# Kernel optimization log

Measured on AMD Instinct MI355X. Metric: run time of the kernel, lower is better.

The kernel has to match this reference:

```python
import jax, jax.numpy as jnp
import numpy as np
from jax import lax

NPOINT = 1024
RADIUS = 0.4
NSAMPLE = 32
EPS = 1e-5


def setup_inputs() -> dict:
    key = jax.random.key(0)
    ks = jax.random.split(key, 8)
    B, N, Cin = 16, 4096, 64
    mlp = [64, 64, 128]
    last = Cin + 3
    inp = {
        "xyz": jax.random.normal(ks[0], (B, N, 3), dtype=jnp.float32),
        "points": jax.random.normal(ks[1], (B, N, Cin), dtype=jnp.float32),
    }
    for i, co in enumerate(mlp):
        inp[f"w{i}"] = jax.random.normal(ks[2 + i], (co, last), dtype=jnp.float32) * 0.05
        inp[f"b{i}"] = jnp.zeros((co,), jnp.float32)
        inp[f"g{i}"] = jnp.ones((co,), jnp.float32)
        inp[f"be{i}"] = jnp.zeros((co,), jnp.float32)
        last = co
    return inp


def _gather(pts, idx):
    # pts: [B, N, C], idx: [B, ...] -> [B, ..., C]
    return jax.vmap(lambda p, i: p[i])(pts, idx)


def farthest_point_sample(xyz, npoint):
    # Deterministic variant: start from index 0 (torch uses a random start).
    B, N, _ = xyz.shape
    bidx = jnp.arange(B)

    def step(carry, _):
        distance, farthest = carry
        centroid = xyz[bidx, farthest][:, None, :]          # [B,1,3]
        dist = jnp.sum((xyz - centroid) ** 2, -1)           # [B,N]
        distance = jnp.minimum(distance, dist)
        return (distance, jnp.argmax(distance, -1)), farthest

    init = (jnp.full((B, N), 1e10, xyz.dtype), jnp.zeros((B,), jnp.int32))
    _, cent = lax.scan(step, init, None, length=npoint)
    return cent.T                                            # [B, npoint]


def query_ball_point(radius, nsample, xyz, new_xyz):
    B, N, _ = xyz.shape
    # [B, S, N] squared distances centroid -> all points
    sqr = jnp.sum((xyz[:, None, :, :] - new_xyz[:, :, None, :]) ** 2, -1)
    gi = jnp.where(sqr > radius ** 2, N, jnp.arange(N)[None, None, :])
    gi = jnp.sort(gi, axis=-1)[:, :, :nsample]               # smallest in-ball indices
    gi = jnp.where(gi == N, gi[:, :, :1], gi)                # pad with first neighbor
    return gi


def reference(xyz, points, w0, b0, g0, be0, w1, b1, g1, be1, w2, b2, g2, be2):
    B, N, _ = xyz.shape
    cent = farthest_point_sample(xyz, NPOINT)                # [B,S]
    new_xyz = _gather(xyz, cent)                             # [B,S,3]
    gi = query_ball_point(RADIUS, NSAMPLE, xyz, new_xyz)     # [B,S,K]
    grouped_xyz = _gather(xyz, gi) - new_xyz[:, :, None, :]  # [B,S,K,3]
    x = jnp.concatenate([grouped_xyz, _gather(points, gi)], -1)  # [B,S,K,3+Cin]
    for w, b, g, be in ((w0, b0, g0, be0), (w1, b1, g1, be1), (w2, b2, g2, be2)):
        x = jnp.einsum('bskc,oc->bsko', x, w) + b            # 1x1 conv
        m = jnp.mean(x, axis=(0, 1, 2))
        v = jnp.var(x, axis=(0, 1, 2))                       # biased var, as torch BN
        x = jax.nn.relu(g * (x - m) * lax.rsqrt(v + EPS) + be)
    new_points = jnp.max(x, axis=2)                          # max over nsample -> [B,S,Cout]
    return new_xyz, new_points
```

## Files before the change

### kernel.cpp

```cpp
#include <hip/hip_runtime.h>
#include <math.h>


static constexpr int BATCH  = 16;
static constexpr int NPTS   = 4096;
static constexpr int NPOINT = 1024;
static constexpr int NSAMP  = 32;
static constexpr int CIN    = 64;
static constexpr int ROWS   = BATCH * NPOINT * NSAMP;
static constexpr int NBLK   = ROWS / 64;

typedef unsigned long long u64;

__device__ __forceinline__ float sqdist(float x, float y, float z,
                                        float cx, float cy, float cz) {
    float dx = x - cx, dy = y - cy, dz = z - cz;
    return __fadd_rn(__fadd_rn(__fmul_rn(dx, dx), __fmul_rn(dy, dy)), __fmul_rn(dz, dz));
}

#if __has_builtin(__builtin_amdgcn_update_dpp) && __has_builtin(__builtin_amdgcn_readlane)
#define DPP_MAX(x, ctrl)                                                              \
    do {                                                                              \
        int _o = __builtin_amdgcn_update_dpp(__float_as_int(x), __float_as_int(x),    \
                                             (ctrl), 0xf, 0xf, false);                \
        (x) = fmaxf((x), __int_as_float(_o));                                         \
    } while (0)
__device__ __forceinline__ float wave_max_f32(float v) {
    DPP_MAX(v, 0x111);
    DPP_MAX(v, 0x112);
    DPP_MAX(v, 0x114);
    DPP_MAX(v, 0x118);
    DPP_MAX(v, 0x142);
    DPP_MAX(v, 0x143);
    return __int_as_float(__builtin_amdgcn_readlane(__float_as_int(v), 63));
}
#else
__device__ __forceinline__ float wave_max_f32(float v) {
#pragma unroll
    for (int m = 1; m < 64; m <<= 1) v = fmaxf(v, __shfl_xor(v, m));
    return v;
}
#endif

__global__ __launch_bounds__(512) void pre_kernel(
    const float* __restrict__ xyz, const float* __restrict__ points,
    const float* __restrict__ w0, const float* __restrict__ b0,
    float* __restrict__ P, float* __restrict__ new_xyz) {
    __shared__ __align__(16) char s_raw[53376];
    const int tid = threadIdx.x;

    if (blockIdx.x < 16) {
        float2* sxy  = (float2*)s_raw;
        float*  szv  = (float*)(s_raw + 32768);
        int*    s_cent = (int*)(s_raw + 49152);
        u64*    s_red  = (u64*)(s_raw + 53248);

        const int b = blockIdx.x;
        const float* xb = xyz + (size_t)b * NPTS * 3;
        for (int p = tid; p < NPTS; p += 512) {
            sxy[p] = make_float2(xb[p * 3 + 0], xb[p * 3 + 1]);
            szv[p] = xb[p * 3 + 2];
        }
        __syncthreads();
        float px[8], py[8], pz[8], dist[8];
#pragma unroll
        for (int j = 0; j < 8; ++j) {
            int p = tid + j * 512;
            float2 f = sxy[p];
            px[j] = f.x; py[j] = f.y; pz[j] = szv[p];
            dist[j] = 1e10f;
        }
        const int lane = tid & 63, wid = tid >> 6;
        int far = 0;
        for (int it = 0; it < NPOINT; ++it) {
            if (tid == 0) s_cent[it] = far;
            const float2 cxy = sxy[far];
            const float  cz  = szv[far];
            float bv = -1.0f;
            int   bi = 0;
#pragma unroll
            for (int j = 0; j < 8; ++j) {
                float d  = sqdist(px[j], py[j], pz[j], cxy.x, cxy.y, cz);
                float nd = fminf(dist[j], d);
                dist[j]  = nd;
                if (nd > bv) { bv = nd; bi = tid + j * 512; }
            }
            float gmax = wave_max_f32(bv);
            u64 mask = __ballot(bv == gmax);
            int widx = __shfl(bi, (int)__builtin_ctzll(mask));
            if (lane == 0)
                s_red[(it & 1) * 8 + wid] =
                    ((u64)__float_as_uint(gmax) << 32) | (unsigned)(4095 - widx);
            __syncthreads();
            const u64* sr = &s_red[(it & 1) * 8];
            u64 w = sr[0];
#pragma unroll
            for (int k = 1; k < 8; ++k) { u64 o = sr[k]; w = (o > w) ? o : w; }
            far = 4095 - (int)(w & 0xffffffffu);
        }
        __syncthreads();
        for (int s = tid; s < NPOINT; s += 512) {
            int c = s_cent[s];
            float2 f = sxy[c];
            new_xyz[((size_t)b * NPOINT + s) * 3 + 0] = f.x;
            new_xyz[((size_t)b * NPOINT + s) * 3 + 1] = f.y;
            new_xyz[((size_t)b * NPOINT + s) * 3 + 2] = szv[c];
        }
    } else {
        float (*xw)[68] = (float(*)[68])s_raw;
        float (*wt)[68] = (float(*)[68])(s_raw + 34816);
        const int blk = blockIdx.x - 16;
        const int pt0 = blk * 128;
        const int ty = tid >> 4, tx = tid & 15;

        for (int idx = tid; idx < 128 * 3; idx += 512) {
            int r = idx / 3, d = idx - r * 3;
            xw[r][d] = xyz[(size_t)(pt0 + r) * 3 + d];
        }
        for (int idx = tid; idx < 128 * 16; idx += 512) {
            int r = idx >> 4, c4 = idx & 15;
            float4 v = *(const float4*)(points + (size_t)(pt0 + r) * CIN + c4 * 4);
            xw[r][3 + c4 * 4 + 0] = v.x;
            xw[r][3 + c4 * 4 + 1] = v.y;
            xw[r][3 + c4 * 4 + 2] = v.z;
            xw[r][3 + c4 * 4 + 3] = v.w;
        }
        for (int idx = tid; idx < 64 * 67; idx += 512) {
            int o = idx / 67, c = idx - o * 67;
            wt[o][c] = w0[idx];
        }
        __syncthreads();

        float acc[4][4];
        {
            float bj[4];
#pragma unroll
            for (int j = 0; j < 4; ++j) bj[j] = b0[tx + 16 * j];
#pragma unroll
            for (int i = 0; i < 4; ++i)
#pragma unroll
                for (int j = 0; j < 4; ++j) acc[i][j] = bj[j];
        }
        for (int c4 = 0; c4 < 64; c4 += 4) {
            float4 xv[4], wv[4];
#pragma unroll
            for (int i = 0; i < 4; ++i) xv[i] = *(const float4*)&xw[ty + 32 * i][c4];
#pragma unroll
            for (int j = 0; j < 4; ++j) wv[j] = *(const float4*)&wt[tx + 16 * j][c4];
#pragma unroll
            for (int i = 0; i < 4; ++i)
#pragma unroll
                for (int j = 0; j < 4; ++j)
                    acc[i][j] += xv[i].x * wv[j].x + xv[i].y * wv[j].y +
                                 xv[i].z * wv[j].z + xv[i].w * wv[j].w;
        }
#pragma unroll
        for (int c = 64; c < 67; ++c) {
            float xv[4], wv[4];
#pragma unroll
            for (int i = 0; i < 4; ++i) xv[i] = xw[ty + 32 * i][c];
#pragma unroll
            for (int j = 0; j < 4; ++j) wv[j] = wt[tx + 16 * j][c];
#pragma unroll
            for (int i = 0; i < 4; ++i)
#pragma unroll
                for (int j = 0; j < 4; ++j) acc[i][j] += xv[i] * wv[j];
        }
#pragma unroll
        for (int i = 0; i < 4; ++i)
#pragma unroll
            for (int j = 0; j < 4; ++j)
                P[(size_t)(pt0 + ty + 32 * i) * 64 + tx + 16 * j] = acc[i][j];
    }
}

__global__ __launch_bounds__(256) void ballq_kernel(const float* __restrict__ xyz,
                                                    const float* __restrict__ new_xyz,
                                                    int* __restrict__ gi) {
    const int lane = threadIdx.x & 63;
    const int w    = threadIdx.x >> 6;
    const int pair = blockIdx.x * 4 + w;
    const int b    = pair >> 10;
    const float R2 = (float)(0.4 * 0.4);
    const float* xb = xyz + (size_t)b * NPTS * 3;
    const float cx = new_xyz[pair * 3 + 0];
    const float cy = new_xyz[pair * 3 + 1];
    const float cz = new_xyz[pair * 3 + 2];
    int* g = gi + (size_t)pair * NSAMP;

    int found = 0, first = 0;
    bool have_first = false;
    for (int c0 = 0; c0 < NPTS; c0 += 64) {
        const int n = c0 + lane;
        float d = sqdist(xb[n * 3 + 0], xb[n * 3 + 1], xb[n * 3 + 2], cx, cy, cz);
        bool in = !(d > R2);
        unsigned long long m = __ballot(in);
        if (m) {
            if (!have_first) { first = c0 + (__ffsll(m) - 1); have_first = true; }
            if (in) {
                int slot = found + (int)__popcll(m & ((1ull << lane) - 1ull));
                if (slot < NSAMP) g[slot] = n;
            }
            found += (int)__popcll(m);
            if (found >= NSAMP) break;
        }
    }
    for (int slot = found + lane; slot < NSAMP; slot += 64) g[slot] = first;
}

__global__ __launch_bounds__(256) void point_q_kernel(const float* __restrict__ new_xyz,
                                                      const float* __restrict__ w0,
                                                      float* __restrict__ Q) {
    int idx = blockIdx.x * 256 + threadIdx.x;
    int s = idx >> 6, o = idx & 63;
    float x = new_xyz[s * 3 + 0], y = new_xyz[s * 3 + 1], z = new_xyz[s * 3 + 2];
    Q[idx] = w0[o * 67 + 0] * x + w0[o * 67 + 1] * y + w0[o * 67 + 2] * z;
}

__global__ __launch_bounds__(256) void stats0_kernel(
    const float* __restrict__ P, const float* __restrict__ Q,
    const int* __restrict__ gi, float* __restrict__ partial) {
    __shared__ __align__(16) float xw[64][68];
    __shared__ int s_n[64];
    const int tid = threadIdx.x, blk = blockIdx.x;
    const int row0 = blk * 64;
    if (tid < 64) s_n[tid] = ((row0 + tid) >> 15) * NPTS + gi[row0 + tid];
    __syncthreads();
    for (int idx = tid; idx < 64 * 16; idx += 256) {
        int r = idx >> 4, c4 = idx & 15;
        float4 pv = *(const float4*)(P + ((size_t)s_n[r] << 6) + c4 * 4);
        float4 qv = *(const float4*)(Q + ((size_t)(blk * 2 + (r >> 5)) << 6) + c4 * 4);
        float4 y; y.x = pv.x - qv.x; y.y = pv.y - qv.y; y.z = pv.z - qv.z; y.w = pv.w - qv.w;
        *(float4*)&xw[r][c4 * 4] = y;
    }
    __syncthreads();
    if (tid < 64) {
        float s = 0.f, q = 0.f;
        for (int r = 0; r < 64; ++r) { float v = xw[r][tid]; s += v; q += v * v; }
        partial[(size_t)blk * 128 + tid]      = s;
        partial[(size_t)blk * 128 + 64 + tid] = q;
    }
}

__global__ __launch_bounds__(256) void chain1_kernel(
    const float* __restrict__ P, const float* __restrict__ Q,
    const int* __restrict__ gi, const float* __restrict__ w1, const float* __restrict__ b1,
    const float* __restrict__ ss, float* __restrict__ partial) {
    __shared__ __align__(16) float xw[64][68];
    __shared__ __align__(16) float wt[64][68];
    __shared__ int s_n[64];
    const int tid = threadIdx.x, blk = blockIdx.x;
    const int row0 = blk * 64;
    const int ty = tid >> 4, tx = tid & 15;

    if (tid < 64) s_n[tid] = ((row0 + tid) >> 15) * NPTS + gi[row0 + tid];
    for (int idx = tid; idx < 64 * 64; idx += 256) {
        int o = idx >> 6, c = idx & 63;
        wt[o][c] = w1[idx];
    }
    __syncthreads();
    for (int idx = tid; idx < 64 * 16; idx += 256) {
        int r = idx >> 4, c4 = idx & 15, c = c4 * 4;
        float4 pv = *(const float4*)(P + ((size_t)s_n[r] << 6) + c);
        float4 qv = *(const float4*)(Q + ((size_t)(blk * 2 + (r >> 5)) << 6) + c);
        float4 y;
        y.x = fmaxf((pv.x - qv.x) * ss[c + 0] + ss[128 + c + 0], 0.f);
        y.y = fmaxf((pv.y - qv.y) * ss[c + 1] + ss[128 + c + 1], 0.f);
        y.z = fmaxf((pv.z - qv.z) * ss[c + 2] + ss[128 + c + 2], 0.f);
        y.w = fmaxf((pv.w - qv.w) * ss[c + 3] + ss[128 + c + 3], 0.f);
        *(float4*)&xw[r][c] = y;
    }
    __syncthreads();

    float acc[4][4];
    {
        float bj[4];
#pragma unroll
        for (int j = 0; j < 4; ++j) bj[j] = b1[tx + 16 * j];
#pragma unroll
        for (int i = 0; i < 4; ++i)
#pragma unroll
            for (int j = 0; j < 4; ++j) acc[i][j] = bj[j];
    }
    for (int c4 = 0; c4 < 64; c4 += 4) {
        float4 xv[4], wv[4];
#pragma unroll
        for (int i = 0; i < 4; ++i) xv[i] = *(const float4*)&xw[ty + 16 * i][c4];
#pragma unroll
        for (int j = 0; j < 4; ++j) wv[j] = *(const float4*)&wt[tx + 16 * j][c4];
#pragma unroll
        for (int i = 0; i < 4; ++i)
#pragma unroll
            for (int j = 0; j < 4; ++j)
                acc[i][j] += xv[i].x * wv[j].x + xv[i].y * wv[j].y +
                             xv[i].z * wv[j].z + xv[i].w * wv[j].w;
    }
    __syncthreads();
#pragma unroll
    for (int i = 0; i < 4; ++i)
#pragma unroll
        for (int j = 0; j < 4; ++j) xw[ty + 16 * i][tx + 16 * j] = acc[i][j];
    __syncthreads();
    if (tid < 64) {
        float s = 0.f, q = 0.f;
        for (int r = 0; r < 64; ++r) { float v = xw[r][tid]; s += v; q += v * v; }
        partial[(size_t)blk * 128 + tid]      = s;
        partial[(size_t)blk * 128 + 64 + tid] = q;
    }
}

__global__ __launch_bounds__(256) void chain2_kernel(
    const float* __restrict__ P, const float* __restrict__ Q,
    const int* __restrict__ gi,
    const float* __restrict__ w1, const float* __restrict__ b1,
    const float* __restrict__ w2, const float* __restrict__ b2,
    const float* __restrict__ ss, float* __restrict__ partial,
    float* __restrict__ maxy) {
    __shared__ __align__(16) float xw[64][68];
    __shared__ __align__(16) float wt[128][68];
    __shared__ int s_n[64];
    const int tid = threadIdx.x, blk = blockIdx.x;
    const int row0 = blk * 64;
    const int ty = tid >> 4, tx = tid & 15;

    if (tid < 64) s_n[tid] = ((row0 + tid) >> 15) * NPTS + gi[row0 + tid];
    for (int idx = tid; idx < 64 * 64; idx += 256) {
        int o = idx >> 6, c = idx & 63;
        wt[o][c] = w1[idx];
    }
    __syncthreads();
    for (int idx = tid; idx < 64 * 16; idx += 256) {
        int r = idx >> 4, c4 = idx & 15, c = c4 * 4;
        float4 pv = *(const float4*)(P + ((size_t)s_n[r] << 6) + c);
        float4 qv = *(const float4*)(Q + ((size_t)(blk * 2 + (r >> 5)) << 6) + c);
        float4 y;
        y.x = fmaxf((pv.x - qv.x) * ss[c + 0] + ss[128 + c + 0], 0.f);
        y.y = fmaxf((pv.y - qv.y) * ss[c + 1] + ss[128 + c + 1], 0.f);
        y.z = fmaxf((pv.z - qv.z) * ss[c + 2] + ss[128 + c + 2], 0.f);
        y.w = fmaxf((pv.w - qv.w) * ss[c + 3] + ss[128 + c + 3], 0.f);
        *(float4*)&xw[r][c] = y;
    }
    __syncthreads();

    float acc[4][4];
    {
        float bj[4];
#pragma unroll
        for (int j = 0; j < 4; ++j) bj[j] = b1[tx + 16 * j];
#pragma unroll
        for (int i = 0; i < 4; ++i)
#pragma unroll
            for (int j = 0; j < 4; ++j) acc[i][j] = bj[j];
    }
    for (int c4 = 0; c4 < 64; c4 += 4) {
        float4 xv[4], wv[4];
#pragma unroll
        for (int i = 0; i < 4; ++i) xv[i] = *(const float4*)&xw[ty + 16 * i][c4];
#pragma unroll
        for (int j = 0; j < 4; ++j) wv[j] = *(const float4*)&wt[tx + 16 * j][c4];
#pragma unroll
        for (int i = 0; i < 4; ++i)
#pragma unroll
            for (int j = 0; j < 4; ++j)
                acc[i][j] += xv[i].x * wv[j].x + xv[i].y * wv[j].y +
                             xv[i].z * wv[j].z + xv[i].w * wv[j].w;
    }
    __syncthreads();
#pragma unroll
    for (int i = 0; i < 4; ++i)
#pragma unroll
        for (int j = 0; j < 4; ++j) {
            int o = tx + 16 * j;
            xw[ty + 16 * i][o] = fmaxf(acc[i][j] * ss[256 + o] + ss[384 + o], 0.f);
        }
    for (int idx = tid; idx < 128 * 64; idx += 256) {
        int o = idx >> 6, c = idx & 63;
        wt[o][c] = w2[idx];
    }
    __syncthreads();

    float acc2[4][8];
    {
        float bj[8];
#pragma unroll
        for (int j = 0; j < 8; ++j) bj[j] = b2[tx + 16 * j];
#pragma unroll
        for (int i = 0; i < 4; ++i)
#pragma unroll
            for (int j = 0; j < 8; ++j) acc2[i][j] = bj[j];
    }
    for (int c4 = 0; c4 < 64; c4 += 4) {
        float4 xv[4], wv[8];
#pragma unroll
        for (int i = 0; i < 4; ++i) xv[i] = *(const float4*)&xw[ty + 16 * i][c4];
#pragma unroll
        for (int j = 0; j < 8; ++j) wv[j] = *(const float4*)&wt[tx + 16 * j][c4];
#pragma unroll
        for (int i = 0; i < 4; ++i)
#pragma unroll
            for (int j = 0; j < 8; ++j)
                acc2[i][j] += xv[i].x * wv[j].x + xv[i].y * wv[j].y +
                              xv[i].z * wv[j].z + xv[i].w * wv[j].w;
    }

    const int bs0 = blk * 2;
#pragma unroll
    for (int half = 0; half < 2; ++half) {
        __syncthreads();
#pragma unroll
        for (int i = 0; i < 4; ++i)
#pragma unroll
            for (int jj = 0; jj < 4; ++jj)
                xw[ty + 16 * i][tx + 16 * jj] = acc2[i][half * 4 + jj];
        __syncthreads();
        if (tid < 64) {
            float s = 0.f, q = 0.f, m0 = -1e30f, m1 = -1e30f;
            for (int r = 0; r < 32; ++r)  { float v = xw[r][tid]; s += v; q += v * v; m0 = fmaxf(m0, v); }
            for (int r = 32; r < 64; ++r) { float v = xw[r][tid]; s += v; q += v * v; m1 = fmaxf(m1, v); }
            int cg = half * 64 + tid;
            partial[(size_t)blk * 256 + cg]       = s;
            partial[(size_t)blk * 256 + 128 + cg] = q;
            maxy[(size_t)bs0 * 128 + cg]          = m0;
            maxy[(size_t)(bs0 + 1) * 128 + cg]    = m1;
        }
    }
}

__global__ __launch_bounds__(256) void reduce_stats_kernel(
    const float* __restrict__ partial, int Cd, float inv_count,
    const float* __restrict__ g, const float* __restrict__ be,
    float* __restrict__ ss_layer) {
    const int c   = blockIdx.x;
    const int tid = threadIdx.x;
    float s = 0.f, q = 0.f;
    for (int blk = tid; blk < NBLK; blk += 256) {
        s += partial[(size_t)blk * 2 * Cd + c];
        q += partial[(size_t)blk * 2 * Cd + Cd + c];
    }
#pragma unroll
    for (int m = 1; m < 64; m <<= 1) { s += __shfl_xor(s, m); q += __shfl_xor(q, m); }
    __shared__ float ls[4], lq[4];
    const int wid = tid >> 6;
    if ((tid & 63) == 0) { ls[wid] = s; lq[wid] = q; }
    __syncthreads();
    if (tid == 0) {
        s = ls[0] + ls[1] + ls[2] + ls[3];
        q = lq[0] + lq[1] + lq[2] + lq[3];
        float mean = s * inv_count;
        float var  = q * inv_count - mean * mean;
        float sc   = g[c] / sqrtf(var + 1e-5f);
        ss_layer[c]       = sc;
        ss_layer[128 + c] = be[c] - mean * sc;
    }
}

__global__ __launch_bounds__(256) void final_kernel(const float* __restrict__ maxy,
                                                    const float* __restrict__ ss2,
                                                    float* __restrict__ outp) {
    int idx = blockIdx.x * 256 + threadIdx.x;
    int c = idx & 127;
    float v = maxy[idx] * ss2[c] + ss2[128 + c];
    outp[idx] = fmaxf(v, 0.f);
}

extern "C" void kernel_launch(void* const* d_in, const int* in_sizes, int n_in,
                              void* d_out, int out_size, void* d_ws, size_t ws_size,
                              hipStream_t stream) {
    const float* xyz    = (const float*)d_in[0];
    const float* points = (const float*)d_in[1];
    const float* w0 = (const float*)d_in[2];  const float* b0  = (const float*)d_in[3];
    const float* g0 = (const float*)d_in[4];  const float* be0 = (const float*)d_in[5];
    const float* w1 = (const float*)d_in[6];  const float* b1  = (const float*)d_in[7];
    const float* g1 = (const float*)d_in[8];  const float* be1 = (const float*)d_in[9];
    const float* w2 = (const float*)d_in[10]; const float* b2  = (const float*)d_in[11];
    const float* g2 = (const float*)d_in[12]; const float* be2 = (const float*)d_in[13];

    float* out      = (float*)d_out;
    float* new_xyz  = out;
    float* out_pts  = out + (size_t)BATCH * NPOINT * 3;

    char* p = (char*)d_ws;
    int* gi = (int*)p;          p += (((size_t)ROWS * 4) + 255) & ~(size_t)255;
    float* partial = (float*)p; p += (((size_t)NBLK * 256 * 4) + 255) & ~(size_t)255;
    float* ss = (float*)p;      p += ((size_t)(3 * 256 * 4) + 255) & ~(size_t)255;
    float* maxy = (float*)p;    p += (((size_t)BATCH * NPOINT * 128 * 4) + 255) & ~(size_t)255;
    float* P = (float*)p;       p += (((size_t)BATCH * NPTS * 64 * 4) + 255) & ~(size_t)255;
    float* Q = (float*)p;

    const float inv_count = 1.0f / (float)ROWS;

    pre_kernel<<<16 + 512, 512, 0, stream>>>(xyz, points, w0, b0, P, new_xyz);
    ballq_kernel<<<(BATCH * NPOINT) / 4, 256, 0, stream>>>(xyz, new_xyz, gi);
    point_q_kernel<<<(BATCH * NPOINT * 64) / 256, 256, 0, stream>>>(new_xyz, w0, Q);

    stats0_kernel<<<NBLK, 256, 0, stream>>>(P, Q, gi, partial);
    reduce_stats_kernel<<<64, 256, 0, stream>>>(partial, 64, inv_count, g0, be0, ss + 0);

    chain1_kernel<<<NBLK, 256, 0, stream>>>(P, Q, gi, w1, b1, ss, partial);
    reduce_stats_kernel<<<64, 256, 0, stream>>>(partial, 64, inv_count, g1, be1, ss + 256);

    chain2_kernel<<<NBLK, 256, 0, stream>>>(P, Q, gi, w1, b1, w2, b2, ss, partial, maxy);
    reduce_stats_kernel<<<128, 256, 0, stream>>>(partial, 128, inv_count, g2, be2, ss + 512);

    final_kernel<<<(BATCH * NPOINT * 128) / 256, 256, 0, stream>>>(maxy, ss + 512, out_pts);
}
```

Measured before the change: 1.073 ms.

## Use bf16 MFMA for MLP chains, barrier-free FPS reduction, fuse Q into ball query

The layer-1 and layer-2 1x1-conv chains now convert activations and weights to bf16 in swizzled shared memory and run them on MFMA 16x16x32 instructions, with the per-channel sum, sum-of-squares and max reduced through shuffles. The farthest-point-sampling loop drops its per-iteration __syncthreads in favour of tagged double-buffered key slots that waves poll, and it passes the winner's coordinates along so the next centroid needs no lookup. The separate point_q kernel is folded into the ball-query kernel. The aim is to cut FP32 ALU time in the chains and the serial barrier latency in FPS. In exchange, bf16 precision can shift the batch-norm statistics, and the spin-wait depends on LDS ordering holding up.

New measurement: 1.573 ms. +46.7%, slower.

```diff
diff --git a/kernel.cpp b/kernel.cpp
--- a/kernel.cpp
+++ b/kernel.cpp
@@ -1,4 +1,5 @@
 #include <hip/hip_runtime.h>
+#include <hip/hip_bf16.h>
 #include <math.h>
 
 
@@ -11,6 +12,8 @@
 static constexpr int NBLK   = ROWS / 64;
 
 typedef unsigned long long u64;
+typedef float f32x4 __attribute__((ext_vector_type(4)));
+typedef short short8v __attribute__((ext_vector_type(8)));
 
 __device__ __forceinline__ float sqdist(float x, float y, float z,
                                         float cx, float cy, float cz) {
@@ -19,44 +22,61 @@
 }
 
 #if __has_builtin(__builtin_amdgcn_update_dpp) && __has_builtin(__builtin_amdgcn_readlane)
-#define DPP_MAX(x, ctrl)                                                              \
+#define DPP_FMAX(x, ctrl)                                                             \
     do {                                                                              \
         int _o = __builtin_amdgcn_update_dpp(__float_as_int(x), __float_as_int(x),    \
                                              (ctrl), 0xf, 0xf, false);                \
         (x) = fmaxf((x), __int_as_float(_o));                                         \
     } while (0)
-__device__ __forceinline__ float wave_max_f32(float v) {
-    DPP_MAX(v, 0x111);
-    DPP_MAX(v, 0x112);
-    DPP_MAX(v, 0x114);
-    DPP_MAX(v, 0x118);
-    DPP_MAX(v, 0x142);
-    DPP_MAX(v, 0x143);
+#define WAVE_RED_F(x) do { DPP_FMAX(x,0x111); DPP_FMAX(x,0x112); DPP_FMAX(x,0x114); \
+                           DPP_FMAX(x,0x118); DPP_FMAX(x,0x142); DPP_FMAX(x,0x143); } while (0)
+__device__ __forceinline__ float bcast63(float v) {
     return __int_as_float(__builtin_amdgcn_readlane(__float_as_int(v), 63));
 }
 #else
-__device__ __forceinline__ float wave_max_f32(float v) {
-#pragma unroll
-    for (int m = 1; m < 64; m <<= 1) v = fmaxf(v, __shfl_xor(v, m));
-    return v;
-}
+#define WAVE_RED_F(x) do { for (int _m = 1; _m < 64; _m <<= 1) (x) = fmaxf((x), __shfl_xor((x), _m)); } while (0)
+__device__ __forceinline__ float bcast63(float v) { return __shfl(v, 63); }
 #endif
+
+__device__ __forceinline__ unsigned short f2bf(float v) {
+    union { __hip_bfloat16 b; unsigned short u; } c;
+    c.b = __float2bfloat16(v);
+    return c.u;
+}
+
+__device__ __forceinline__ int swz(int row, int bir) {
+    return (row << 7) | (bir ^ ((row & 7) << 4));
+}
+
+__device__ __forceinline__ short8v load_frag(const char* b, int row, int k0) {
+    union { uint2 v; short s[4]; } lo, hi;
+    lo.v = *(const uint2*)(b + swz(row, 2 * k0));
+    hi.v = *(const uint2*)(b + swz(row, 2 * k0 + 32));
+    short8v f;
+    f[0] = lo.s[0]; f[1] = lo.s[1]; f[2] = lo.s[2]; f[3] = lo.s[3];
+    f[4] = hi.s[0]; f[5] = hi.s[1]; f[6] = hi.s[2]; f[7] = hi.s[3];
+    return f;
+}
 
 __global__ __launch_bounds__(512) void pre_kernel(
     const float* __restrict__ xyz, const float* __restrict__ points,
     const float* __restrict__ w0, const float* __restrict__ b0,
     float* __restrict__ P, float* __restrict__ new_xyz) {
-    __shared__ __align__(16) char s_raw[53376];
+    __shared__ __align__(16) char s_raw[53568];
     const int tid = threadIdx.x;
 
     if (blockIdx.x < 16) {
-        float2* sxy  = (float2*)s_raw;
-        float*  szv  = (float*)(s_raw + 32768);
+        float2* sxy    = (float2*)s_raw;
+        float*  szv    = (float*)(s_raw + 32768);
         int*    s_cent = (int*)(s_raw + 49152);
-        u64*    s_red  = (u64*)(s_raw + 53248);
+        u64*    s_key  = (u64*)(s_raw + 53248);
+        float*  s_cx   = (float*)(s_raw + 53376);
+        float*  s_cy   = (float*)(s_raw + 53440);
+        float*  s_cz   = (float*)(s_raw + 53504);
 
         const int b = blockIdx.x;
         const float* xb = xyz + (size_t)b * NPTS * 3;
+        if (tid < 16) s_key[tid] = 0x3FFull;
         for (int p = tid; p < NPTS; p += 512) {
             sxy[p] = make_float2(xb[p * 3 + 0], xb[p * 3 + 1]);
             szv[p] = xb[p * 3 + 2];
@@ -72,31 +92,64 @@
         }
         const int lane = tid & 63, wid = tid >> 6;
         int far = 0;
+        float2 c0 = sxy[0];
+        float cx = c0.x, cy = c0.y, cz = szv[0];
         for (int it = 0; it < NPOINT; ++it) {
             if (tid == 0) s_cent[it] = far;
-            const float2 cxy = sxy[far];
-            const float  cz  = szv[far];
             float bv = -1.0f;
             int   bi = 0;
+            float bx = 0.f, by = 0.f, bz = 0.f;
 #pragma unroll
             for (int j = 0; j < 8; ++j) {
-                float d  = sqdist(px[j], py[j], pz[j], cxy.x, cxy.y, cz);
+                float d  = sqdist(px[j], py[j], pz[j], cx, cy, cz);
                 float nd = fminf(dist[j], d);
                 dist[j]  = nd;
-                if (nd > bv) { bv = nd; bi = tid + j * 512; }
+                bool gt = (nd > bv);
+                bv = gt ? nd : bv;  bi = gt ? (tid + j * 512) : bi;
+                bx = gt ? px[j] : bx; by = gt ? py[j] : by; bz = gt ? pz[j] : bz;
             }
-            float gmax = wave_max_f32(bv);
+            float red = bv;
+            WAVE_RED_F(red);
+            float gmax = bcast63(red);
             u64 mask = __ballot(bv == gmax);
-            int widx = __shfl(bi, (int)__builtin_ctzll(mask));
-            if (lane == 0)
-                s_red[(it & 1) * 8 + wid] =
-                    ((u64)__float_as_uint(gmax) << 32) | (unsigned)(4095 - widx);
-            __syncthreads();
-            const u64* sr = &s_red[(it & 1) * 8];
-            u64 w = sr[0];
-#pragma unroll
-            for (int k = 1; k < 8; ++k) { u64 o = sr[k]; w = (o > w) ? o : w; }
-            far = 4095 - (int)(w & 0xffffffffu);
+            int win = (int)__builtin_ctzll(mask);
+            const int buf = (it & 1);
+            const u64 tag = (u64)(it & 1023);
+            if (lane == win) {
+                volatile float* vcx = s_cx + buf * 8 + wid;
+                volatile float* vcy = s_cy + buf * 8 + wid;
+                volatile float* vcz = s_cz + buf * 8 + wid;
+                *vcx = bx; *vcy = by; *vcz = bz;
+                __asm__ __volatile__("s_waitcnt lgkmcnt(0)" ::: "memory");
+                *(volatile u64*)(s_key + buf * 8 + wid) =
+                    ((u64)__float_as_uint(bv) << 22) | ((u64)(4095 - bi) << 10) | tag;
+            }
+            volatile u64* sk = s_key + buf * 8;
+            u64 k0, k1, k2, k3, k4, k5, k6, k7;
+            do {
+                k0 = sk[0]; k1 = sk[1]; k2 = sk[2]; k3 = sk[3];
+                k4 = sk[4]; k5 = sk[5]; k6 = sk[6]; k7 = sk[7];
+            } while ((((k0 ^ tag) | (k1 ^ tag)) | ((k2 ^ tag) | (k3 ^ tag)) |
+                      ((k4 ^ tag) | (k5 ^ tag)) | ((k6 ^ tag) | (k7 ^ tag))) & 0x3FFull);
+            __asm__ __volatile__("" ::: "memory");
+            const float* pcx = s_cx + buf * 8;
+            const float* pcy = s_cy + buf * 8;
+            const float* pcz = s_cz + buf * 8;
+            float4 x01 = *(const float4*)pcx,       x23 = *(const float4*)(pcx + 4);
+            float4 y01 = *(const float4*)pcy,       y23 = *(const float4*)(pcy + 4);
+            float4 z01 = *(const float4*)pcz,       z23 = *(const float4*)(pcz + 4);
+            u64 wk = k0; float fx = x01.x, fy = y01.x, fz = z01.x;
+#define SEL(ki, xc, yc, zc) if ((ki) > wk) { wk = (ki); fx = (xc); fy = (yc); fz = (zc); }
+            SEL(k1, x01.y, y01.y, z01.y)
+            SEL(k2, x01.z, y01.z, z01.z)
+            SEL(k3, x01.w, y01.w, z01.w)
+            SEL(k4, x23.x, y23.x, z23.x)
+            SEL(k5, x23.y, y23.y, z23.y)
+            SEL(k6, x23.z, y23.z, z23.z)
+            SEL(k7, x23.w, y23.w, z23.w)
+#undef SEL
+            far = 4095 - (int)((wk >> 10) & 0xFFFull);
+            cx = fx; cy = fy; cz = fz;
         }
         __syncthreads();
         for (int s = tid; s < NPOINT; s += 512) {
@@ -176,7 +229,9 @@
 
 __global__ __launch_bounds__(256) void ballq_kernel(const float* __restrict__ xyz,
                                                     const float* __restrict__ new_xyz,
-                                                    int* __restrict__ gi) {
+                                                    const float* __restrict__ w0,
+                                                    int* __restrict__ gi,
+                                                    float* __restrict__ Q) {
     const int lane = threadIdx.x & 63;
     const int w    = threadIdx.x >> 6;
     const int pair = blockIdx.x * 4 + w;
@@ -187,6 +242,9 @@
     const float cy = new_xyz[pair * 3 + 1];
     const float cz = new_xyz[pair * 3 + 2];
     int* g = gi + (size_t)pair * NSAMP;
+
+    Q[(size_t)pair * 64 + lane] =
+        w0[lane * 67 + 0] * cx + w0[lane * 67 + 1] * cy + w0[lane * 67 + 2] * cz;
 
     int found = 0, first = 0;
     bool have_first = false;
@@ -208,15 +266,6 @@
     for (int slot = found + lane; slot < NSAMP; slot += 64) g[slot] = first;
 }
 
-__global__ __launch_bounds__(256) void point_q_kernel(const float* __restrict__ new_xyz,
-                                                      const float* __restrict__ w0,
-                                                      float* __restrict__ Q) {
-    int idx = blockIdx.x * 256 + threadIdx.x;
-    int s = idx >> 6, o = idx & 63;
-    float x = new_xyz[s * 3 + 0], y = new_xyz[s * 3 + 1], z = new_xyz[s * 3 + 2];
-    Q[idx] = w0[o * 67 + 0] * x + w0[o * 67 + 1] * y + w0[o * 67 + 2] * z;
-}
-
 __global__ __launch_bounds__(256) void stats0_kernel(
     const float* __restrict__ P, const float* __restrict__ Q,
     const int* __restrict__ gi, float* __restrict__ partial) {
@@ -242,187 +291,171 @@
     }
 }
 
-__global__ __launch_bounds__(256) void chain1_kernel(
+
+__global__ __launch_bounds__(256) void chainM1_kernel(
     const float* __restrict__ P, const float* __restrict__ Q,
     const int* __restrict__ gi, const float* __restrict__ w1, const float* __restrict__ b1,
     const float* __restrict__ ss, float* __restrict__ partial) {
-    __shared__ __align__(16) float xw[64][68];
-    __shared__ __align__(16) float wt[64][68];
+    __shared__ __align__(16) char h0b[64 * 128];
+    __shared__ __align__(16) char w1b[64 * 128];
+    __shared__ float sredS[4][64], sredQ[4][64];
     __shared__ int s_n[64];
     const int tid = threadIdx.x, blk = blockIdx.x;
     const int row0 = blk * 64;
-    const int ty = tid >> 4, tx = tid & 15;
-
     if (tid < 64) s_n[tid] = ((row0 + tid) >> 15) * NPTS + gi[row0 + tid];
-    for (int idx = tid; idx < 64 * 64; idx += 256) {
-        int o = idx >> 6, c = idx & 63;
-        wt[o][c] = w1[idx];
-    }
-    __syncthreads();
-    for (int idx = tid; idx < 64 * 16; idx += 256) {
-        int r = idx >> 4, c4 = idx & 15, c = c4 * 4;
-        float4 pv = *(const float4*)(P + ((size_t)s_n[r] << 6) + c);
-        float4 qv = *(const float4*)(Q + ((size_t)(blk * 2 + (r >> 5)) << 6) + c);
-        float4 y;
-        y.x = fmaxf((pv.x - qv.x) * ss[c + 0] + ss[128 + c + 0], 0.f);
-        y.y = fmaxf((pv.y - qv.y) * ss[c + 1] + ss[128 + c + 1], 0.f);
-        y.z = fmaxf((pv.z - qv.z) * ss[c + 2] + ss[128 + c + 2], 0.f);
-        y.w = fmaxf((pv.w - qv.w) * ss[c + 3] + ss[128 + c + 3], 0.f);
-        *(float4*)&xw[r][c] = y;
-    }
-    __syncthreads();
-
-    float acc[4][4];
-    {
-        float bj[4];
-#pragma unroll
-        for (int j = 0; j < 4; ++j) bj[j] = b1[tx + 16 * j];
-#pragma unroll
-        for (int i = 0; i < 4; ++i)
-#pragma unroll
-            for (int j = 0; j < 4; ++j) acc[i][j] = bj[j];
-    }
-    for (int c4 = 0; c4 < 64; c4 += 4) {
-        float4 xv[4], wv[4];
-#pragma unroll
-        for (int i = 0; i < 4; ++i) xv[i] = *(const float4*)&xw[ty + 16 * i][c4];
-#pragma unroll
-        for (int j = 0; j < 4; ++j) wv[j] = *(const float4*)&wt[tx + 16 * j][c4];
-#pragma unroll
-        for (int i = 0; i < 4; ++i)
-#pragma unroll
-            for (int j = 0; j < 4; ++j)
-                acc[i][j] += xv[i].x * wv[j].x + xv[i].y * wv[j].y +
-                             xv[i].z * wv[j].z + xv[i].w * wv[j].w;
-    }
-    __syncthreads();
-#pragma unroll
-    for (int i = 0; i < 4; ++i)
-#pragma unroll
-        for (int j = 0; j < 4; ++j) xw[ty + 16 * i][tx + 16 * j] = acc[i][j];
+    for (int idx = tid; idx < 1024; idx += 256) {
+        float4 v = *(const float4*)(w1 + idx * 4);
+        uint2 pk; pk.x = (unsigned)f2bf(v.x) | ((unsigned)f2bf(v.y) << 16);
+        pk.y = (unsigned)f2bf(v.z) | ((unsigned)f2bf(v.w) << 16);
+        *(uint2*)(w1b + swz(idx >> 4, 8 * (idx & 15))) = pk;
+    }
+    __syncthreads();
+    for (int idx = tid; idx < 1024; idx += 256) {
+        int r = idx >> 4, c0 = (idx & 15) * 4;
+        float4 pv = *(const float4*)(P + ((size_t)s_n[r] << 6) + c0);
+        float4 qv = *(const float4*)(Q + ((size_t)(blk * 2 + (r >> 5)) << 6) + c0);
+        float4 sc = *(const float4*)(ss + c0);
+        float4 sh = *(const float4*)(ss + 128 + c0);
+        float y0 = fmaxf((pv.x - qv.x) * sc.x + sh.x, 0.f);
+        float y1v = fmaxf((pv.y - qv.y) * sc.y + sh.y, 0.f);
+        float y2v = fmaxf((pv.z - qv.z) * sc.z + sh.z, 0.f);
+        float y3 = fmaxf((pv.w - qv.w) * sc.w + sh.w, 0.f);
+        uint2 pk; pk.x = (unsigned)f2bf(y0) | ((unsigned)f2bf(y1v) << 16);
+        pk.y = (unsigned)f2bf(y2v) | ((unsigned)f2bf(y3) << 16);
+        *(uint2*)(h0b + swz(r, 8 * (idx & 15))) = pk;
+    }
+    __syncthreads();
+
+    const int l = tid & 63, w = tid >> 6;
+    const int mrow = 16 * w + (l & 15);
+    const int klane = (l >> 4) * 4;
+    short8v a0 = load_frag(h0b, mrow, klane);
+    short8v a1 = load_frag(h0b, mrow, klane + 32);
+#pragma unroll
+    for (int nt = 0; nt < 4; ++nt) {
+        float bias = b1[16 * nt + (l & 15)];
+        f32x4 acc; acc[0] = bias; acc[1] = bias; acc[2] = bias; acc[3] = bias;
+        short8v bA = load_frag(w1b, 16 * nt + (l & 15), klane);
+        short8v bB = load_frag(w1b, 16 * nt + (l & 15), klane + 32);
+        acc = __builtin_amdgcn_mfma_f32_16x16x32_bf16(a0, bA, acc, 0, 0, 0);
+        acc = __builtin_amdgcn_mfma_f32_16x16x32_bf16(a1, bB, acc, 0, 0, 0);
+        float s = acc[0] + acc[1] + acc[2] + acc[3];
+        float q = acc[0] * acc[0] + acc[1] * acc[1] + acc[2] * acc[2] + acc[3] * acc[3];
+        s += __shfl_xor(s, 16); s += __shfl_xor(s, 32);
+        q += __shfl_xor(q, 16); q += __shfl_xor(q, 32);
+        if (l < 16) { sredS[w][nt * 16 + l] = s; sredQ[w][nt * 16 + l] = q; }
+    }
     __syncthreads();
     if (tid < 64) {
-        float s = 0.f, q = 0.f;
-        for (int r = 0; r < 64; ++r) { float v = xw[r][tid]; s += v; q += v * v; }
+        float s = sredS[0][tid] + sredS[1][tid] + sredS[2][tid] + sredS[3][tid];
+        float q = sredQ[0][tid] + sredQ[1][tid] + sredQ[2][tid] + sredQ[3][tid];
         partial[(size_t)blk * 128 + tid]      = s;
         partial[(size_t)blk * 128 + 64 + tid] = q;
     }
 }
 
-__global__ __launch_bounds__(256) void chain2_kernel(
+__global__ __launch_bounds__(256) void chainM2_kernel(
     const float* __restrict__ P, const float* __restrict__ Q,
     const int* __restrict__ gi,
     const float* __restrict__ w1, const float* __restrict__ b1,
     const float* __restrict__ w2, const float* __restrict__ b2,
     const float* __restrict__ ss, float* __restrict__ partial,
     float* __restrict__ maxy) {
-    __shared__ __align__(16) float xw[64][68];
-    __shared__ __align__(16) float wt[128][68];
+    __shared__ __align__(16) char h0b[64 * 128];
+    __shared__ __align__(16) char w1b[64 * 128];
+    __shared__ __align__(16) char h1b[64 * 128];
+    __shared__ __align__(16) char w2b[128 * 128];
+    __shared__ float sredS[4][128], sredQ[4][128], sredM[4][128];
     __shared__ int s_n[64];
     const int tid = threadIdx.x, blk = blockIdx.x;
     const int row0 = blk * 64;
-    const int ty = tid >> 4, tx = tid & 15;
-
     if (tid < 64) s_n[tid] = ((row0 + tid) >> 15) * NPTS + gi[row0 + tid];
-    for (int idx = tid; idx < 64 * 64; idx += 256) {
-        int o = idx >> 6, c = idx & 63;
-        wt[o][c] = w1[idx];
-    }
-    __syncthreads();
-    for (int idx = tid; idx < 64 * 16; idx += 256) {
-        int r = idx >> 4, c4 = idx & 15, c = c4 * 4;
-        float4 pv = *(const float4*)(P + ((size_t)s_n[r] << 6) + c);
-        float4 qv = *(const float4*)(Q + ((size_t)(blk * 2 + (r >> 5)) << 6) + c);
-        float4 y;
-        y.x = fmaxf((pv.x - qv.x) * ss[c + 0] + ss[128 + c + 0], 0.f);
-        y.y = fmaxf((pv.y - qv.y) * ss[c + 1] + ss[128 + c + 1], 0.f);
-        y.z = fmaxf((pv.z - qv.z) * ss[c + 2] + ss[128 + c + 2], 0.f);
-        y.w = fmaxf((pv.w - qv.w) * ss[c + 3] + ss[128 + c + 3], 0.f);
-        *(float4*)&xw[r][c] = y;
-    }
-    __syncthreads();
-
-    float acc[4][4];
+    for (int idx = tid; idx < 1024; idx += 256) {
+        float4 v = *(const float4*)(w1 + idx * 4);
+        uint2 pk; pk.x = (unsigned)f2bf(v.x) | ((unsigned)f2bf(v.y) << 16);
+        pk.y = (unsigned)f2bf(v.z) | ((unsigned)f2bf(v.w) << 16);
+        *(uint2*)(w1b + swz(idx >> 4, 8 * (idx & 15))) = pk;
+    }
+    for (int idx = tid; idx < 2048; idx += 256) {
+        float4 v = *(const float4*)(w2 + idx * 4);
+        uint2 pk; pk.x = (unsigned)f2bf(v.x) | ((unsigned)f2bf(v.y) << 16);
+        pk.y = (unsigned)f2bf(v.z) | ((unsigned)f2bf(v.w) << 16);
+        *(uint2*)(w2b + swz(idx >> 4, 8 * (idx & 15))) = pk;
+    }
+    __syncthreads();
+    for (int idx = tid; idx < 1024; idx += 256) {
+        int r = idx >> 4, c0 = (idx & 15) * 4;
+        float4 pv = *(const float4*)(P + ((size_t)s_n[r] << 6) + c0);
+        float4 qv = *(const float4*)(Q + ((size_t)(blk * 2 + (r >> 5)) << 6) + c0);
+        float4 sc = *(const float4*)(ss + c0);
+        float4 sh = *(const float4*)(ss + 128 + c0);
+        float y0 = fmaxf((pv.x - qv.x) * sc.x + sh.x, 0.f);
+        float y1v = fmaxf((pv.y - qv.y) * sc.y + sh.y, 0.f);
+        float y2v = fmaxf((pv.z - qv.z) * sc.z + sh.z, 0.f);
+        float y3 = fmaxf((pv.w - qv.w) * sc.w + sh.w, 0.f);
+        uint2 pk; pk.x = (unsigned)f2bf(y0) | ((unsigned)f2bf(y1v) << 16);
+        pk.y = (unsigned)f2bf(y2v) | ((unsigned)f2bf(y3) << 16);
+        *(uint2*)(h0b + swz(r, 8 * (idx & 15))) = pk;
+    }
+    __syncthreads();
+
+    const int l = tid & 63, w = tid >> 6;
+    const int mrow = 16 * w + (l & 15);
+    const int klane = (l >> 4) * 4;
     {
-        float bj[4];
-#pragma unroll
-        for (int j = 0; j < 4; ++j) bj[j] = b1[tx + 16 * j];
-#pragma unroll
-        for (int i = 0; i < 4; ++i)
-#pragma unroll
-            for (int j = 0; j < 4; ++j) acc[i][j] = bj[j];
-    }
-    for (int c4 = 0; c4 < 64; c4 += 4) {
-        float4 xv[4], wv[4];
-#pragma unroll
-        for (int i = 0; i < 4; ++i) xv[i] = *(const float4*)&xw[ty + 16 * i][c4];
-#pragma unroll
-        for (int j = 0; j < 4; ++j) wv[j] = *(const float4*)&wt[tx + 16 * j][c4];
-#pragma unroll
-        for (int i = 0; i < 4; ++i)
-#pragma unroll
-            for (int j = 0; j < 4; ++j)
-                acc[i][j] += xv[i].x * wv[j].x + xv[i].y * wv[j].y +
-                             xv[i].z * wv[j].z + xv[i].w * wv[j].w;
-    }
-    __syncthreads();
-#pragma unroll
-    for (int i = 0; i < 4; ++i)
-#pragma unroll
-        for (int j = 0; j < 4; ++j) {
-            int o = tx + 16 * j;
-            xw[ty + 16 * i][o] = fmaxf(acc[i][j] * ss[256 + o] + ss[384 + o], 0.f);
-        }
-    for (int idx = tid; idx < 128 * 64; idx += 256) {
-        int o = idx >> 6, c = idx & 63;
-        wt[o][c] = w2[idx];
-    }
-    __syncthreads();
-
-    float acc2[4][8];
+        short8v a0 = load_frag(h0b, mrow, klane);
+        short8v a1 = load_frag(h0b, mrow, klane + 32);
+#pragma unroll
+        for (int nt = 0; nt < 4; ++nt) {
+            float bias = b1[16 * nt + (l & 15)];
+            f32x4 acc; acc[0] = bias; acc[1] = bias; acc[2] = bias; acc[3] = bias;
+            short8v bA = load_frag(w1b, 16 * nt + (l & 15), klane);
+            short8v bB = load_frag(w1b, 16 * nt + (l & 15), klane + 32);
+            acc = __builtin_amdgcn_mfma_f32_16x16x32_bf16(a0, bA, acc, 0, 0, 0);
+            acc = __builtin_amdgcn_mfma_f32_16x16x32_bf16(a1, bB, acc, 0, 0, 0);
+#pragma unroll
+            for (int p = 0; p < 4; ++p) {
+                int row = 16 * w + (l >> 4) * 4 + p;
+                int col = 16 * nt + (l & 15);
+                float v = fmaxf(acc[p] * ss[256 + col] + ss[384 + col], 0.f);
+                *(unsigned short*)(h1b + swz(row, 2 * col)) = f2bf(v);
+            }
+        }
+    }
+    __syncthreads();
     {
-        float bj[8];
-#pragma unroll
-        for (int j = 0; j < 8; ++j) bj[j] = b2[tx + 16 * j];
-#pragma unroll
-        for (int i = 0; i < 4; ++i)
-#pragma unroll
-            for (int j = 0; j < 8; ++j) acc2[i][j] = bj[j];
-    }
-    for (int c4 = 0; c4 < 64; c4 += 4) {
-        float4 xv[4], wv[8];
-#pragma unroll
-        for (int i = 0; i < 4; ++i) xv[i] = *(const float4*)&xw[ty + 16 * i][c4];
-#pragma unroll
-        for (int j = 0; j < 8; ++j) wv[j] = *(const float4*)&wt[tx + 16 * j][c4];
-#pragma unroll
-        for (int i = 0; i < 4; ++i)
-#pragma unroll
-            for (int j = 0; j < 8; ++j)
-                acc2[i][j] += xv[i].x * wv[j].x + xv[i].y * wv[j].y +
-                              xv[i].z * wv[j].z + xv[i].w * wv[j].w;
-    }
-
-    const int bs0 = blk * 2;
-#pragma unroll
-    for (int half = 0; half < 2; ++half) {
-        __syncthreads();
-#pragma unroll
-        for (int i = 0; i < 4; ++i)
-#pragma unroll
-            for (int jj = 0; jj < 4; ++jj)
-                xw[ty + 16 * i][tx + 16 * jj] = acc2[i][half * 4 + jj];
-        __syncthreads();
-        if (tid < 64) {
-            float s = 0.f, q = 0.f, m0 = -1e30f, m1 = -1e30f;
-            for (int r = 0; r < 32; ++r)  { float v = xw[r][tid]; s += v; q += v * v; m0 = fmaxf(m0, v); }
-            for (int r = 32; r < 64; ++r) { float v = xw[r][tid]; s += v; q += v * v; m1 = fmaxf(m1, v); }
-            int cg = half * 64 + tid;
-            partial[(size_t)blk * 256 + cg]       = s;
-            partial[(size_t)blk * 256 + 128 + cg] = q;
-            maxy[(size_t)bs0 * 128 + cg]          = m0;
-            maxy[(size_t)(bs0 + 1) * 128 + cg]    = m1;
-        }
+        short8v a0 = load_frag(h1b, mrow, klane);
+        short8v a1 = load_frag(h1b, mrow, klane + 32);
+#pragma unroll
+        for (int nt = 0; nt < 8; ++nt) {
+            float bias = b2[16 * nt + (l & 15)];
+            f32x4 acc; acc[0] = bias; acc[1] = bias; acc[2] = bias; acc[3] = bias;
+            short8v bA = load_frag(w2b, 16 * nt + (l & 15), klane);
+            short8v bB = load_frag(w2b, 16 * nt + (l & 15), klane + 32);
+            acc = __builtin_amdgcn_mfma_f32_16x16x32_bf16(a0, bA, acc, 0, 0, 0);
+            acc = __builtin_amdgcn_mfma_f32_16x16x32_bf16(a1, bB, acc, 0, 0, 0);
+            float s = acc[0] + acc[1] + acc[2] + acc[3];
+            float q = acc[0] * acc[0] + acc[1] * acc[1] + acc[2] * acc[2] + acc[3] * acc[3];
+            float m = fmaxf(fmaxf(acc[0], acc[1]), fmaxf(acc[2], acc[3]));
+            s += __shfl_xor(s, 16); s += __shfl_xor(s, 32);
+            q += __shfl_xor(q, 16); q += __shfl_xor(q, 32);
+            m = fmaxf(m, __shfl_xor(m, 16)); m = fmaxf(m, __shfl_xor(m, 32));
+            if (l < 16) {
+                sredS[w][nt * 16 + l] = s;
+                sredQ[w][nt * 16 + l] = q;
+                sredM[w][nt * 16 + l] = m;
+            }
+        }
+    }
+    __syncthreads();
+    if (tid < 128) {
+        float s = sredS[0][tid] + sredS[1][tid] + sredS[2][tid] + sredS[3][tid];
+        float q = sredQ[0][tid] + sredQ[1][tid] + sredQ[2][tid] + sredQ[3][tid];
+        partial[(size_t)blk * 256 + tid]       = s;
+        partial[(size_t)blk * 256 + 128 + tid] = q;
+        const int bs0 = blk * 2;
+        maxy[(size_t)bs0 * 128 + tid]       = fmaxf(sredM[0][tid], sredM[1][tid]);
+        maxy[(size_t)(bs0 + 1) * 128 + tid] = fmaxf(sredM[2][tid], sredM[3][tid]);
     }
 }
 
@@ -490,16 +523,15 @@
     const float inv_count = 1.0f / (float)ROWS;
 
     pre_kernel<<<16 + 512, 512, 0, stream>>>(xyz, points, w0, b0, P, new_xyz);
-    ballq_kernel<<<(BATCH * NPOINT) / 4, 256, 0, stream>>>(xyz, new_xyz, gi);
-    point_q_kernel<<<(BATCH * NPOINT * 64) / 256, 256, 0, stream>>>(new_xyz, w0, Q);
+    ballq_kernel<<<(BATCH * NPOINT) / 4, 256, 0, stream>>>(xyz, new_xyz, w0, gi, Q);
 
     stats0_kernel<<<NBLK, 256, 0, stream>>>(P, Q, gi, partial);
     reduce_stats_kernel<<<64, 256, 0, stream>>>(partial, 64, inv_count, g0, be0, ss + 0);
 
-    chain1_kernel<<<NBLK, 256, 0, stream>>>(P, Q, gi, w1, b1, ss, partial);
+    chainM1_kernel<<<NBLK, 256, 0, stream>>>(P, Q, gi, w1, b1, ss, partial);
     reduce_stats_kernel<<<64, 256, 0, stream>>>(partial, 64, inv_count, g1, be1, ss + 256);
 
-    chain2_kernel<<<NBLK, 256, 0, stream>>>(P, Q, gi, w1, b1, w2, b2, ss, partial, maxy);
+    chainM2_kernel<<<NBLK, 256, 0, stream>>>(P, Q, gi, w1, b1, w2, b2, ss, partial, maxy);
     reduce_stats_kernel<<<128, 256, 0, stream>>>(partial, 128, inv_count, g2, be2, ss + 512);
 
     final_kernel<<<(BATCH * NPOINT * 128) / 256, 256, 0, stream>>>(maxy, ss + 512, out_pts);
```
